# Performance work log

Hardware: AMD Instinct MI355X
Metric: run time of the kernel (lower is better)

The kernel has to match this reference:

```python
import jax, jax.numpy as jnp
import numpy as np

N = 524288      # total trajectory tokens
D_MODEL = 256
HIDDEN = 512
OUT_DIM = 32
N_TYPES = 4


def setup_inputs() -> dict:
    key = jax.random.key(0)
    k1, k2, k3, k4 = jax.random.split(key, 4)
    x = jax.random.normal(k1, (N, D_MODEL), dtype=jnp.float32)
    types = jax.random.randint(k2, (N,), 0, N_TYPES, dtype=jnp.int64)
    W1 = jax.random.normal(k3, (N_TYPES, D_MODEL, HIDDEN), dtype=jnp.float32) / np.sqrt(D_MODEL)
    b1 = jnp.zeros((N_TYPES, HIDDEN), dtype=jnp.float32)
    W2 = jax.random.normal(k4, (N_TYPES, HIDDEN, OUT_DIM), dtype=jnp.float32) / np.sqrt(HIDDEN)
    b2 = jnp.zeros((N_TYPES, OUT_DIM), dtype=jnp.float32)
    return {"x": x, "types": types, "W1": W1, "b1": b1, "W2": W2, "b2": b2}


def reference(x, types, W1, b1, W2, b2):
    # Type-masked gather -> per-type MLP decode -> scatter back to original order.
    # The gather/argsort-scatter of the torch code is equivalent (for equal
    # per-type output dims) to computing each type's decoder and selecting the
    # rows where types == type_id; we loop over the small fixed set of types.
    n_types = W1.shape[0]
    out = jnp.zeros((x.shape[0], W2.shape[-1]), dtype=x.dtype)
    for t in range(n_types):
        h = jax.nn.relu(x @ W1[t] + b1[t])          # [N, HIDDEN]
        y = h @ W2[t] + b2[t]                        # [N, OUT_DIM]
        out = jnp.where((types == t)[:, None], y, out)
    return out
```

## Files before the change

kernel.cpp:

```cpp
#include <hip/hip_runtime.h>
#include <hip/hip_bf16.h>
#include <hip/hip_fp16.h>

#define N_TOK 524288
#define DM 256
#define HID 512
#define OUTD 32
#define NTYPE 4
#define BM 128
#define MT 2
#define HC 32
#define NCHUNK (HID / HC)
#define CHUNK_BYTES (HC * DM * 2)
#define NBLK 512
#define GX1D (N_TOK / BM + NTYPE)

typedef _Float16 half8 __attribute__((ext_vector_type(8)));
typedef float f32x4 __attribute__((ext_vector_type(4)));

#define AS1 __attribute__((address_space(1)))
#define AS3 __attribute__((address_space(3)))


__global__ void count_kernel(const int* __restrict__ types, int* __restrict__ bc) {
    __shared__ int c[NTYPE];
    int tid = threadIdx.x;
    if (tid < NTYPE) c[tid] = 0;
    __syncthreads();
    int b = blockIdx.x;
    int lane = tid & 63;
    #pragma unroll
    for (int j = 0; j < 4; ++j) {
        int t = types[b * 1024 + j * 256 + tid];
        #pragma unroll
        for (int tt = 0; tt < NTYPE; ++tt) {
            unsigned long long mask = __ballot(t == tt);
            if (lane == 0) atomicAdd(&c[tt], __popcll(mask));
        }
    }
    __syncthreads();
    if (tid < NTYPE) bc[tid * NBLK + b] = c[tid];
}

__global__ void scan_blocks_kernel(const int* __restrict__ bc,
                                   int* __restrict__ bb,
                                   int* __restrict__ meta) {
    __shared__ int totals[NTYPE];
    __shared__ int typeoff[NTYPE];
    int wave = threadIdx.x >> 6, lane = threadIdx.x & 63;
    int excl[NBLK / 64];
    int running = 0;
    #pragma unroll
    for (int it = 0; it < NBLK / 64; ++it) {
        int v = bc[wave * NBLK + it * 64 + lane];
        int s = v;
        #pragma unroll
        for (int d = 1; d < 64; d <<= 1) {
            int u = __shfl_up(s, d);
            if (lane >= d) s += u;
        }
        excl[it] = running + s - v;
        running += __shfl(s, 63);
    }
    if (lane == 0) totals[wave] = running;
    __syncthreads();
    if (threadIdx.x == 0) {
        int off = 0, toff = 0;
        for (int tt = 0; tt < NTYPE; ++tt) {
            typeoff[tt] = off;
            meta[tt] = totals[tt];
            meta[4 + tt] = off;
            meta[8 + tt] = toff;
            off += totals[tt];
            toff += (totals[tt] + BM - 1) / BM;
        }
        meta[12] = toff;
    }
    __syncthreads();
    #pragma unroll
    for (int it = 0; it < NBLK / 64; ++it)
        bb[wave * NBLK + it * 64 + lane] = typeoff[wave] + excl[it];
}

__global__ void scatter2_kernel(const int* __restrict__ types,
                                const int* __restrict__ bb,
                                int* __restrict__ idx) {
    __shared__ int base[NTYPE];
    __shared__ int wcnt[4][NTYPE];
    int b = blockIdx.x;
    int tid = threadIdx.x, wave = tid >> 6, lane = tid & 63;
    if (tid < NTYPE) base[tid] = bb[tid * NBLK + b];
    #pragma unroll
    for (int j = 0; j < 4; ++j) {
        __syncthreads();
        int i = b * 1024 + j * 256 + tid;
        int t = types[i];
        int rank = 0;
        #pragma unroll
        for (int tt = 0; tt < NTYPE; ++tt) {
            unsigned long long mask = __ballot(t == tt);
            if (t == tt) rank = __popcll(mask & ((1ull << lane) - 1ull));
            if (lane == 0) wcnt[wave][tt] = __popcll(mask);
        }
        __syncthreads();
        int pre = 0;
        for (int w = 0; w < wave; ++w) pre += wcnt[w][t];
        idx[base[t] + pre + rank] = i;
        __syncthreads();
        if (tid < NTYPE) {
            int tot = 0;
            #pragma unroll
            for (int w = 0; w < 4; ++w) tot += wcnt[w][tid];
            base[tid] += tot;
        }
    }
}


__global__ void wprep_kernel(const float* __restrict__ W1, const float* __restrict__ W2,
                             _Float16* __restrict__ W1T, _Float16* __restrict__ W2T) {
    int i = blockIdx.x * blockDim.x + threadIdx.x;
    if (i < NTYPE * HID * DM) {
        int t = i / (HID * DM);
        int r = i - t * (HID * DM);
        int byteoff = r * 2;
        int hc = byteoff / CHUNK_BYTES;
        int rem = byteoff - hc * CHUNK_BYTES;
        int hr = rem >> 9;
        int brow = rem & 511;
        int d = (brow ^ ((hr & 7) << 4)) >> 1;
        int h = hc * HC + hr;
        W1T[i] = (_Float16)W1[(t * DM + d) * HID + h];
    }
    if (i < NTYPE * OUTD * HID) {
        int t = i / (OUTD * HID);
        int r = i - t * (OUTD * HID);
        int o = r / HID;
        int pg = r - o * HID;
        int hc = pg >> 5;
        int p = pg & 31;
        int lg = p >> 3, j = p & 7;
        int h1 = (j < 4) ? (lg * 4 + j) : (16 + lg * 4 + (j - 4));
        int h = hc * HC + h1;
        W2T[i] = (_Float16)W2[(t * HID + h) * OUTD + o];
    }
}


__launch_bounds__(256)
__global__ void fused_mlp_kernel(const float* __restrict__ x,
                                 const int* __restrict__ meta,
                                 const int* __restrict__ idx,
                                 const _Float16* __restrict__ W1T,
                                 const _Float16* __restrict__ W2T,
                                 const float* __restrict__ b1,
                                 const float* __restrict__ b2,
                                 float* __restrict__ out) {
    const int b = blockIdx.x;
    if (b >= meta[12]) return;
    const int t = (b >= meta[9]) + (b >= meta[10]) + (b >= meta[11]);
    const int cnt = meta[t];
    const int row_base = (b - meta[8 + t]) * BM;
    const int* idx_t = idx + meta[4 + t];

    __shared__ __align__(16) char W1sB[2][CHUNK_BYTES];
    __shared__ __align__(16) float b1s[HID];

    const int tid = threadIdx.x;
    const int wave = tid >> 6;
    const int lane = tid & 63;
    const int l15 = lane & 15;
    const int lg = lane >> 4;

    {
        float2 bv = *(const float2*)(b1 + t * HID + tid * 2);
        b1s[tid * 2] = bv.x;
        b1s[tid * 2 + 1] = bv.y;
    }
    __builtin_amdgcn_sched_barrier(0);

    int rg[32];
    #pragma unroll
    for (int r = 0; r < 32; ++r)
        rg[r] = idx_t[min(row_base + wave * 32 + r, cnt - 1)];
    __builtin_amdgcn_sched_barrier(0);

    half8 afrag[MT][8];
    char* scratch = &W1sB[0][0] + wave * 8192;

#define ISSUE_GROUP(G)                                                          \
    {                                                                           \
        _Pragma("unroll")                                                       \
        for (int i = 0; i < 4; ++i) {                                           \
            const char* src = (const char*)(x + (size_t)rg[(G) * 4 + i] * DM)   \
                              + ((lane - i) & 63) * 16;                         \
            __builtin_amdgcn_global_load_lds(                                   \
                (const AS1 void*)src,                                           \
                (AS3 void*)(scratch + ((G) & 1) * 4096 + i * 1024), 16, 0, 0);  \
        }                                                                       \
    }

    ISSUE_GROUP(0)
#define GATHER_GROUP(G)                                                         \
    {                                                                           \
        if ((G) < 7) { __builtin_amdgcn_sched_barrier(0); ISSUE_GROUP((G) + 1) }\
        if ((G) < 7) asm volatile("s_waitcnt vmcnt(4)");                        \
        else         asm volatile("s_waitcnt vmcnt(0)");                        \
        __builtin_amdgcn_sched_barrier(0);                                      \
        if ((l15 >> 2) == ((G) & 3)) {                                          \
            const int r3 = l15 & 3;                                             \
            const char* gb = scratch + ((G) & 1) * 4096 + r3 * 1024;            \
            _Pragma("unroll")                                                   \
            for (int kk = 0; kk < 8; ++kk) {                                    \
                int B0 = kk * 128 + lg * 32;                                    \
                f32x4 v0 = *(const f32x4*)(gb + ((B0 + r3 * 16) & 1023));       \
                f32x4 v1 = *(const f32x4*)(gb + ((B0 + 16 + r3 * 16) & 1023));  \
                half8 h;                                                        \
                h[0] = (_Float16)v0[0]; h[1] = (_Float16)v0[1];                 \
                h[2] = (_Float16)v0[2]; h[3] = (_Float16)v0[3];                 \
                h[4] = (_Float16)v1[0]; h[5] = (_Float16)v1[1];                 \
                h[6] = (_Float16)v1[2]; h[7] = (_Float16)v1[3];                 \
                afrag[(G) >> 2][kk] = h;                                        \
            }                                                                   \
        }                                                                       \
    }

    GATHER_GROUP(0) GATHER_GROUP(1) GATHER_GROUP(2) GATHER_GROUP(3)
    GATHER_GROUP(4) GATHER_GROUP(5) GATHER_GROUP(6) GATHER_GROUP(7)
#undef GATHER_GROUP
#undef ISSUE_GROUP

    __syncthreads();

    const f32x4 fzero = {0.f, 0.f, 0.f, 0.f};
    f32x4 acc2[MT][2];
    #pragma unroll
    for (int mt = 0; mt < MT; ++mt)
        #pragma unroll
        for (int nt = 0; nt < 2; ++nt)
            acc2[mt][nt] = fzero;

    const char* w1base = (const char*)(W1T + (size_t)t * HID * DM);
    const _Float16* w2t_t = W2T + (size_t)t * OUTD * HID;

    #pragma unroll
    for (int it = 0; it < 4; ++it) {
        __builtin_amdgcn_global_load_lds(
            (const AS1 void*)(w1base + it * 4096 + tid * 16),
            (AS3 void*)(&W1sB[0][it * 4096 + tid * 16]),
            16, 0, 0);
    }
    half8 w2A[2], w2B[2];
    #pragma unroll
    for (int nt = 0; nt < 2; ++nt)
        w2A[nt] = *(const half8*)(w2t_t + (nt * 16 + l15) * HID + lg * 8);
    __syncthreads();

#define CHUNK_BODY(HCI, W2USE, W2FILL)                                          \
    {                                                                           \
        const int hc = (HCI);                                                   \
        const char* cur = W1sB[hc & 1];                                         \
        if (hc + 1 < NCHUNK) {                                                  \
            const char* src = w1base + (size_t)(hc + 1) * CHUNK_BYTES;          \
            char* dst = W1sB[(hc + 1) & 1];                                     \
            _Pragma("unroll")                                                   \
            for (int it = 0; it < 4; ++it) {                                    \
                __builtin_amdgcn_global_load_lds(                               \
                    (const AS1 void*)(src + it * 4096 + tid * 16),              \
                    (AS3 void*)(dst + it * 4096 + tid * 16),                    \
                    16, 0, 0);                                                  \
            }                                                                   \
        }                                                                       \
        {                 \
            int hn = (hc + 1) & 15;                                             \
            _Pragma("unroll")                                                   \
            for (int nt = 0; nt < 2; ++nt)                                      \
                W2FILL[nt] = *(const half8*)(w2t_t + (nt * 16 + l15) * HID + hn * HC + lg * 8); \
        }                                                                       \
        f32x4 acc1[MT][2];    \
        _Pragma("unroll")                                                       \
        for (int mt = 0; mt < MT; ++mt)                                         \
            _Pragma("unroll")                                                   \
            for (int nt = 0; nt < 2; ++nt)                                      \
                acc1[mt][nt] = fzero;                                           \
        _Pragma("unroll")                                                       \
        for (int kk = 0; kk < 8; ++kk) {                                        \
            half8 bfr[2];                                                       \
            _Pragma("unroll")                                                   \
            for (int nt = 0; nt < 2; ++nt) {                                    \
                int hr = nt * 16 + l15;                                         \
                bfr[nt] = *(const half8*)(cur + hr * 512 +                      \
                            ((kk * 64 + lg * 16) ^ ((hr & 7) << 4)));           \
            }                                                                   \
            _Pragma("unroll")                                                   \
            for (int mt = 0; mt < MT; ++mt)                                     \
                _Pragma("unroll")                                               \
                for (int nt = 0; nt < 2; ++nt)                                  \
                    acc1[mt][nt] = __builtin_amdgcn_mfma_f32_16x16x32_f16(      \
                        bfr[nt], afrag[mt][kk], acc1[mt][nt], 0, 0, 0);         \
        }                                                                       \
              \
        {                                                                       \
            f32x4 bv0 = *(const f32x4*)(b1s + hc * HC + lg * 4);                \
            f32x4 bv1 = *(const f32x4*)(b1s + hc * HC + 16 + lg * 4);           \
            _Pragma("unroll")                                                   \
            for (int mt = 0; mt < MT; ++mt) {                                   \
                half8 hfrag;                                                    \
                _Pragma("unroll")                                               \
                for (int j = 0; j < 4; ++j) {                                   \
                    hfrag[j]     = (_Float16)fmaxf(acc1[mt][0][j] + bv0[j], 0.f);\
                    hfrag[4 + j] = (_Float16)fmaxf(acc1[mt][1][j] + bv1[j], 0.f);\
                }                                                               \
                _Pragma("unroll")                                               \
                for (int nt = 0; nt < 2; ++nt)                                  \
                    acc2[mt][nt] = __builtin_amdgcn_mfma_f32_16x16x32_f16(      \
                        W2USE[nt], hfrag, acc2[mt][nt], 0, 0, 0);               \
            }                                                                   \
        }                                                                       \
        __syncthreads();   \
    }

    #pragma unroll
    for (int h2 = 0; h2 < NCHUNK; h2 += 2) {
        CHUNK_BODY(h2, w2A, w2B);
        CHUNK_BODY(h2 + 1, w2B, w2A);
    }
#undef CHUNK_BODY

    const int m = min(BM, cnt - row_base);
    f32x4 b2v[2];
    #pragma unroll
    for (int nt = 0; nt < 2; ++nt)
        b2v[nt] = *(const f32x4*)(b2 + t * OUTD + nt * 16 + lg * 4);
    #pragma unroll
    for (int mt = 0; mt < MT; ++mt) {
        int rloc = wave * (MT * 16) + mt * 16 + l15;
        if (rloc < m) {
            int gr = idx_t[row_base + rloc];
            #pragma unroll
            for (int nt = 0; nt < 2; ++nt) {
                f32x4 v = acc2[mt][nt] + b2v[nt];
                __builtin_nontemporal_store(v, (f32x4*)(out + (size_t)gr * OUTD + nt * 16 + lg * 4));
            }
        }
    }
}


extern "C" void kernel_launch(void* const* d_in, const int* in_sizes, int n_in,
                              void* d_out, int out_size, void* d_ws, size_t ws_size,
                              hipStream_t stream) {
    const float* x   = (const float*)d_in[0];
    const int* types = (const int*)d_in[1];
    const float* W1  = (const float*)d_in[2];
    const float* b1  = (const float*)d_in[3];
    const float* W2  = (const float*)d_in[4];
    const float* b2  = (const float*)d_in[5];
    float* out = (float*)d_out;

    char* ws = (char*)d_ws;
    int* meta = (int*)ws;
    int* idx = (int*)(ws + 64);
    _Float16* W1T = (_Float16*)(ws + 64 + 4 * (size_t)N_TOK);
    _Float16* W2T = W1T + (size_t)NTYPE * HID * DM;
    int* bc = (int*)W1T;
    int* bb = bc + NTYPE * NBLK;

    count_kernel<<<NBLK, 256, 0, stream>>>(types, bc);
    scan_blocks_kernel<<<1, 256, 0, stream>>>(bc, bb, meta);
    scatter2_kernel<<<NBLK, 256, 0, stream>>>(types, bb, idx);
    wprep_kernel<<<(NTYPE * HID * DM) / 256, 256, 0, stream>>>(W1, W2, W1T, W2T);

    fused_mlp_kernel<<<GX1D, 256, 0, stream>>>(x, meta, idx, W1T, W2T, b1, b2, out);
}
```

Before: 233.4 us.

## Triple-buffer W1 chunks with two-ahead prefetch and partial vmcnt waits

Expands the LDS buffer for W1 chunks from two to three and prefetches two chunks ahead instead of one. The full __syncthreads at the end of each chunk is replaced by a partial s_waitcnt vmcnt plus s_barrier, so only the next chunk's loads must complete and later loads stay in flight. W2 register loads are reordered ahead of the W1 prefetch, with sched_barriers pinning the order. The aim is to hide global-to-LDS latency, at the cost of extra LDS that may lower occupancy and of hand-counted vmcnt values that must match the actual number of outstanding loads.

```diff
diff --git a/kernel.cpp b/kernel.cpp
--- a/kernel.cpp
+++ b/kernel.cpp
@@ -163,7 +163,7 @@
     const int row_base = (b - meta[8 + t]) * BM;
     const int* idx_t = idx + meta[4 + t];
 
-    __shared__ __align__(16) char W1sB[2][CHUNK_BYTES];
+    __shared__ __align__(16) char W1sB[3][CHUNK_BYTES];
     __shared__ __align__(16) float b1s[HID];
 
     const int tid = threadIdx.x;
@@ -243,46 +243,51 @@
     const char* w1base = (const char*)(W1T + (size_t)t * HID * DM);
     const _Float16* w2t_t = W2T + (size_t)t * OUTD * HID;
 
-    #pragma unroll
-    for (int it = 0; it < 4; ++it) {
+    half8 w2A[2], w2B[2];
+    #pragma unroll
+    for (int nt = 0; nt < 2; ++nt)
+        w2A[nt] = *(const half8*)(w2t_t + (nt * 16 + l15) * HID + lg * 8);
+    #pragma unroll
+    for (int it = 0; it < 4; ++it)
         __builtin_amdgcn_global_load_lds(
             (const AS1 void*)(w1base + it * 4096 + tid * 16),
-            (AS3 void*)(&W1sB[0][it * 4096 + tid * 16]),
-            16, 0, 0);
-    }
-    half8 w2A[2], w2B[2];
-    #pragma unroll
-    for (int nt = 0; nt < 2; ++nt)
-        w2A[nt] = *(const half8*)(w2t_t + (nt * 16 + l15) * HID + lg * 8);
+            (AS3 void*)(&W1sB[0][it * 4096 + tid * 16]), 16, 0, 0);
+    #pragma unroll
+    for (int it = 0; it < 4; ++it)
+        __builtin_amdgcn_global_load_lds(
+            (const AS1 void*)(w1base + CHUNK_BYTES + it * 4096 + tid * 16),
+            (AS3 void*)(&W1sB[1][it * 4096 + tid * 16]), 16, 0, 0);
     __syncthreads();
 
 #define CHUNK_BODY(HCI, W2USE, W2FILL)                                          \
     {                                                                           \
         const int hc = (HCI);                                                   \
-        const char* cur = W1sB[hc & 1];                                         \
+               \
         if (hc + 1 < NCHUNK) {                                                  \
-            const char* src = w1base + (size_t)(hc + 1) * CHUNK_BYTES;          \
-            char* dst = W1sB[(hc + 1) & 1];                                     \
-            _Pragma("unroll")                                                   \
-            for (int it = 0; it < 4; ++it) {                                    \
+            _Pragma("unroll")                                                   \
+            for (int nt = 0; nt < 2; ++nt)                                      \
+                W2FILL[nt] = *(const half8*)(w2t_t + (nt * 16 + l15) * HID      \
+                                             + (hc + 1) * HC + lg * 8);         \
+        }                                                                       \
+        __builtin_amdgcn_sched_barrier(0);                                      \
+                                 \
+        if (hc + 2 < NCHUNK) {                                                  \
+            const char* srcw = w1base + (size_t)(hc + 2) * CHUNK_BYTES;         \
+            char* dstw = W1sB[(hc + 2) % 3];                                    \
+            _Pragma("unroll")                                                   \
+            for (int it = 0; it < 4; ++it)                                      \
                 __builtin_amdgcn_global_load_lds(                               \
-                    (const AS1 void*)(src + it * 4096 + tid * 16),              \
-                    (AS3 void*)(dst + it * 4096 + tid * 16),                    \
-                    16, 0, 0);                                                  \
-            }                                                                   \
-        }                                                                       \
-        {                 \
-            int hn = (hc + 1) & 15;                                             \
-            _Pragma("unroll")                                                   \
-            for (int nt = 0; nt < 2; ++nt)                                      \
-                W2FILL[nt] = *(const half8*)(w2t_t + (nt * 16 + l15) * HID + hn * HC + lg * 8); \
-        }                                                                       \
+                    (const AS1 void*)(srcw + it * 4096 + tid * 16),             \
+                    (AS3 void*)(dstw + it * 4096 + tid * 16), 16, 0, 0);        \
+        }                                                                       \
+        __builtin_amdgcn_sched_barrier(0);                                      \
         f32x4 acc1[MT][2];    \
         _Pragma("unroll")                                                       \
         for (int mt = 0; mt < MT; ++mt)                                         \
             _Pragma("unroll")                                                   \
             for (int nt = 0; nt < 2; ++nt)                                      \
                 acc1[mt][nt] = fzero;                                           \
+        const char* cur = W1sB[hc % 3];                                         \
         _Pragma("unroll")                                                       \
         for (int kk = 0; kk < 8; ++kk) {                                        \
             half8 bfr[2];                                                       \
@@ -317,7 +322,16 @@
                         W2USE[nt], hfrag, acc2[mt][nt], 0, 0, 0);               \
             }                                                                   \
         }                                                                       \
-        __syncthreads();   \
+           \
+        if (hc < 14) {                                                          \
+            asm volatile("s_waitcnt vmcnt(6)");                                 \
+            __builtin_amdgcn_sched_barrier(0);                                  \
+            __builtin_amdgcn_s_barrier();                                       \
+        } else if (hc == 14) {                                                  \
+            asm volatile("s_waitcnt vmcnt(2)");                                 \
+            __builtin_amdgcn_sched_barrier(0);                                  \
+            __builtin_amdgcn_s_barrier();                                       \
+        }                            \
     }
 
     #pragma unroll
```

New measurement: 269.5 us. +15.5%, slower.

## Use single-wave blocks reading fragment-ordered W1 directly from global memory

Applied to the files above, without the earlier changes.

Replaces the 4-wave, 128-row blocks that staged W1 chunks through double-buffered LDS with single-wave, 32-row blocks. Each wave now loads W1 B-fragments straight from global memory, which wprep pre-permutes into MFMA fragment order. The bias is also read from global memory. This removes all block-level barriers and most LDS use, which should raise occupancy. In exchange, each block reuses its W1 reads across only 32 rows, so W1 traffic from L2 rises about fourfold, and there are four times as many blocks.

```diff
diff --git a/kernel.cpp b/kernel.cpp
--- a/kernel.cpp
+++ b/kernel.cpp
@@ -7,13 +7,12 @@
 #define HID 512
 #define OUTD 32
 #define NTYPE 4
-#define BM 128
+#define TBM 32
 #define MT 2
 #define HC 32
 #define NCHUNK (HID / HC)
-#define CHUNK_BYTES (HC * DM * 2)
 #define NBLK 512
-#define GX1D (N_TOK / BM + NTYPE)
+#define GX1D (N_TOK / TBM + NTYPE)
 
 typedef _Float16 half8 __attribute__((ext_vector_type(8)));
 typedef float f32x4 __attribute__((ext_vector_type(4)));
@@ -72,7 +71,7 @@
             meta[4 + tt] = off;
             meta[8 + tt] = toff;
             off += totals[tt];
-            toff += (totals[tt] + BM - 1) / BM;
+            toff += (totals[tt] + TBM - 1) / TBM;
         }
         meta[12] = toff;
     }
@@ -118,19 +117,23 @@
 
 
 __global__ void wprep_kernel(const float* __restrict__ W1, const float* __restrict__ W2,
-                             _Float16* __restrict__ W1T, _Float16* __restrict__ W2T) {
+                             _Float16* __restrict__ W1F, _Float16* __restrict__ W2T) {
     int i = blockIdx.x * blockDim.x + threadIdx.x;
     if (i < NTYPE * HID * DM) {
         int t = i / (HID * DM);
-        int r = i - t * (HID * DM);
-        int byteoff = r * 2;
-        int hc = byteoff / CHUNK_BYTES;
-        int rem = byteoff - hc * CHUNK_BYTES;
-        int hr = rem >> 9;
-        int brow = rem & 511;
-        int d = (brow ^ ((hr & 7) << 4)) >> 1;
-        int h = hc * HC + hr;
-        W1T[i] = (_Float16)W1[(t * DM + d) * HID + h];
+        int slot = i - t * (HID * DM);
+        int hc = slot >> 13;
+        int rem = slot & 8191;
+        int kk = rem >> 10;
+        int rem2 = rem & 1023;
+        int nt = rem2 >> 9;
+        int rem3 = rem2 & 511;
+        int lane = rem3 >> 3;
+        int j = rem3 & 7;
+        int lg = lane >> 4, l15 = lane & 15;
+        int h = hc * HC + nt * 16 + l15;
+        int d = kk * 32 + lg * 8 + j;
+        W1F[i] = (_Float16)W1[(t * DM + d) * HID + h];
     }
     if (i < NTYPE * OUTD * HID) {
         int t = i / (OUTD * HID);
@@ -147,11 +150,11 @@
 }
 
 
-__launch_bounds__(256)
+__launch_bounds__(64, 4)
 __global__ void fused_mlp_kernel(const float* __restrict__ x,
                                  const int* __restrict__ meta,
                                  const int* __restrict__ idx,
-                                 const _Float16* __restrict__ W1T,
+                                 const _Float16* __restrict__ W1F,
                                  const _Float16* __restrict__ W2T,
                                  const float* __restrict__ b1,
                                  const float* __restrict__ b2,
@@ -160,33 +163,22 @@
     if (b >= meta[12]) return;
     const int t = (b >= meta[9]) + (b >= meta[10]) + (b >= meta[11]);
     const int cnt = meta[t];
-    const int row_base = (b - meta[8 + t]) * BM;
+    const int row_base = (b - meta[8 + t]) * TBM;
     const int* idx_t = idx + meta[4 + t];
 
-    __shared__ __align__(16) char W1sB[2][CHUNK_BYTES];
-    __shared__ __align__(16) float b1s[HID];
-
-    const int tid = threadIdx.x;
-    const int wave = tid >> 6;
-    const int lane = tid & 63;
+    __shared__ __align__(16) char scratch[8192];
+
+    const int lane = threadIdx.x & 63;
     const int l15 = lane & 15;
     const int lg = lane >> 4;
 
-    {
-        float2 bv = *(const float2*)(b1 + t * HID + tid * 2);
-        b1s[tid * 2] = bv.x;
-        b1s[tid * 2 + 1] = bv.y;
-    }
+    int rg[32];
+    #pragma unroll
+    for (int r = 0; r < 32; ++r)
+        rg[r] = idx_t[min(row_base + r, cnt - 1)];
     __builtin_amdgcn_sched_barrier(0);
 
-    int rg[32];
-    #pragma unroll
-    for (int r = 0; r < 32; ++r)
-        rg[r] = idx_t[min(row_base + wave * 32 + r, cnt - 1)];
-    __builtin_amdgcn_sched_barrier(0);
-
     half8 afrag[MT][8];
-    char* scratch = &W1sB[0][0] + wave * 8192;
 
 #define ISSUE_GROUP(G)                                                          \
     {                                                                           \
@@ -196,7 +188,8 @@
                               + ((lane - i) & 63) * 16;                         \
             __builtin_amdgcn_global_load_lds(                                   \
                 (const AS1 void*)src,                                           \
-                (AS3 void*)(scratch + ((G) & 1) * 4096 + i * 1024), 16, 0, 0);  \
+                (AS3 void*)(scratch + ((G) & 1) * 4096 + i * 1024 + lane * 16), \
+                16, 0, 0);                                                      \
         }                                                                       \
     }
 
@@ -230,8 +223,6 @@
 #undef GATHER_GROUP
 #undef ISSUE_GROUP
 
-    __syncthreads();
-
     const f32x4 fzero = {0.f, 0.f, 0.f, 0.f};
     f32x4 acc2[MT][2];
     #pragma unroll
@@ -240,37 +231,18 @@
         for (int nt = 0; nt < 2; ++nt)
             acc2[mt][nt] = fzero;
 
-    const char* w1base = (const char*)(W1T + (size_t)t * HID * DM);
+    const _Float16* w1f = W1F + (size_t)t * HID * DM;
     const _Float16* w2t_t = W2T + (size_t)t * OUTD * HID;
-
-    #pragma unroll
-    for (int it = 0; it < 4; ++it) {
-        __builtin_amdgcn_global_load_lds(
-            (const AS1 void*)(w1base + it * 4096 + tid * 16),
-            (AS3 void*)(&W1sB[0][it * 4096 + tid * 16]),
-            16, 0, 0);
-    }
+    const float* b1t = b1 + t * HID;
+
     half8 w2A[2], w2B[2];
     #pragma unroll
     for (int nt = 0; nt < 2; ++nt)
         w2A[nt] = *(const half8*)(w2t_t + (nt * 16 + l15) * HID + lg * 8);
-    __syncthreads();
 
 #define CHUNK_BODY(HCI, W2USE, W2FILL)                                          \
     {                                                                           \
         const int hc = (HCI);                                                   \
-        const char* cur = W1sB[hc & 1];                                         \
-        if (hc + 1 < NCHUNK) {                                                  \
-            const char* src = w1base + (size_t)(hc + 1) * CHUNK_BYTES;          \
-            char* dst = W1sB[(hc + 1) & 1];                                     \
-            _Pragma("unroll")                                                   \
-            for (int it = 0; it < 4; ++it) {                                    \
-                __builtin_amdgcn_global_load_lds(                               \
-                    (const AS1 void*)(src + it * 4096 + tid * 16),              \
-                    (AS3 void*)(dst + it * 4096 + tid * 16),                    \
-                    16, 0, 0);                                                  \
-            }                                                                   \
-        }                                                                       \
         {                 \
             int hn = (hc + 1) & 15;                                             \
             _Pragma("unroll")                                                   \
@@ -283,15 +255,13 @@
             _Pragma("unroll")                                                   \
             for (int nt = 0; nt < 2; ++nt)                                      \
                 acc1[mt][nt] = fzero;                                           \
+        const _Float16* wchunk = w1f + (size_t)hc * 8192;                       \
         _Pragma("unroll")                                                       \
         for (int kk = 0; kk < 8; ++kk) {                                        \
             half8 bfr[2];                                                       \
             _Pragma("unroll")                                                   \
-            for (int nt = 0; nt < 2; ++nt) {                                    \
-                int hr = nt * 16 + l15;                                         \
-                bfr[nt] = *(const half8*)(cur + hr * 512 +                      \
-                            ((kk * 64 + lg * 16) ^ ((hr & 7) << 4)));           \
-            }                                                                   \
+            for (int nt = 0; nt < 2; ++nt)                                      \
+                bfr[nt] = *(const half8*)(wchunk + kk * 1024 + nt * 512 + lane * 8); \
             _Pragma("unroll")                                                   \
             for (int mt = 0; mt < MT; ++mt)                                     \
                 _Pragma("unroll")                                               \
@@ -301,8 +271,8 @@
         }                                                                       \
               \
         {                                                                       \
-            f32x4 bv0 = *(const f32x4*)(b1s + hc * HC + lg * 4);                \
-            f32x4 bv1 = *(const f32x4*)(b1s + hc * HC + 16 + lg * 4);           \
+            f32x4 bv0 = *(const f32x4*)(b1t + hc * HC + lg * 4);                \
+            f32x4 bv1 = *(const f32x4*)(b1t + hc * HC + 16 + lg * 4);           \
             _Pragma("unroll")                                                   \
             for (int mt = 0; mt < MT; ++mt) {                                   \
                 half8 hfrag;                                                    \
@@ -317,7 +287,6 @@
                         W2USE[nt], hfrag, acc2[mt][nt], 0, 0, 0);               \
             }                                                                   \
         }                                                                       \
-        __syncthreads();   \
     }
 
     #pragma unroll
@@ -327,14 +296,14 @@
     }
 #undef CHUNK_BODY
 
-    const int m = min(BM, cnt - row_base);
+    const int m = min(TBM, cnt - row_base);
     f32x4 b2v[2];
     #pragma unroll
     for (int nt = 0; nt < 2; ++nt)
         b2v[nt] = *(const f32x4*)(b2 + t * OUTD + nt * 16 + lg * 4);
     #pragma unroll
     for (int mt = 0; mt < MT; ++mt) {
-        int rloc = wave * (MT * 16) + mt * 16 + l15;
+        int rloc = mt * 16 + l15;
         if (rloc < m) {
             int gr = idx_t[row_base + rloc];
             #pragma unroll
@@ -361,15 +330,15 @@
     char* ws = (char*)d_ws;
     int* meta = (int*)ws;
     int* idx = (int*)(ws + 64);
-    _Float16* W1T = (_Float16*)(ws + 64 + 4 * (size_t)N_TOK);
-    _Float16* W2T = W1T + (size_t)NTYPE * HID * DM;
-    int* bc = (int*)W1T;
+    _Float16* W1F = (_Float16*)(ws + 64 + 4 * (size_t)N_TOK);
+    _Float16* W2T = W1F + (size_t)NTYPE * HID * DM;
+    int* bc = (int*)W1F;
     int* bb = bc + NTYPE * NBLK;
 
     count_kernel<<<NBLK, 256, 0, stream>>>(types, bc);
     scan_blocks_kernel<<<1, 256, 0, stream>>>(bc, bb, meta);
     scatter2_kernel<<<NBLK, 256, 0, stream>>>(types, bb, idx);
-    wprep_kernel<<<(NTYPE * HID * DM) / 256, 256, 0, stream>>>(W1, W2, W1T, W2T);
-
-    fused_mlp_kernel<<<GX1D, 256, 0, stream>>>(x, meta, idx, W1T, W2T, b1, b2, out);
-}
+    wprep_kernel<<<(NTYPE * HID * DM) / 256, 256, 0, stream>>>(W1, W2, W1F, W2T);
+
+    fused_mlp_kernel<<<GX1D, 64, 0, stream>>>(x, meta, idx, W1F, W2T, b1, b2, out);
+}
```

Result: slower. 370.6 us (+58.8%).
